# Kernel tuning notes

Measured on AMD Instinct MI355X. Metric: run time of the kernel, lower is better.

Reference implementation:

```python
import jax, jax.numpy as jnp
import numpy as np

T_BINS = 1000  # max_time_bins
N_HEADS = 8
BIN = 64


def _ln(x, g, b):
    m = x.mean(-1, keepdims=True)
    v = ((x - m) ** 2).mean(-1, keepdims=True)
    return (x - m) / jnp.sqrt(v + 1e-5) * g + b


def _time_attn(h, td, mask, wq, bq, wk, bk, wv, bv, wo, bo, temb):
    # h: [B,S,D], td: [B,S] float, mask: [B,S] bool
    B, S, D = h.shape
    dk = D // N_HEADS
    q = (h @ wq + bq).reshape(B, S, N_HEADS, dk)
    k = (h @ wk + bk).reshape(B, S, N_HEADS, dk)
    v = (h @ wv + bv).reshape(B, S, N_HEADS, dk)
    scores = jnp.einsum('bqhd,bkhd->bhqk', q, k) / jnp.sqrt(jnp.float32(dk))
    tb = jnp.clip(td.astype(jnp.int32), 0, T_BINS - 1)
    bias = temb[tb].transpose(0, 2, 1)[:, :, None, :]  # [B,H,1,S], key-position bias
    scores = jnp.where(mask[:, None, None, :], scores + bias, -1e9)
    attn = jax.nn.softmax(scores, axis=-1)
    ctx = jnp.einsum('bhqk,bkhd->bqhd', attn, v).reshape(B, S, D)
    return ctx @ wo + bo


def _forward(x, time_deltas,
             emb_event, emb_rel, emb_abs,
             iq_w, iq_b, ik_w, ik_b, iv_w, iv_b, io_w, io_b, i_temb, i_g, i_bt,
             eq_w, eq_b, ek_w, ek_b, ev_w, ev_b, eo_w, eo_b, e_temb, e_g, e_bt,
             w1, b1, w2, b2):
    B, S = x.shape
    NB = S // BIN  # S chosen as a multiple of bin_size -> no padding
    mask = x != 0  # padding_idx = 0
    ee = emb_event.at[0].set(0.0)  # padding_idx row is zero
    rel_bins = jnp.clip(time_deltas.astype(jnp.int32), 0, T_BINS - 1)
    abs_t = jnp.cumsum(jnp.clip(time_deltas, 0.0, None), axis=1)
    abs_bins = jnp.clip(abs_t.astype(jnp.int32), 0, T_BINS - 1)
    h = ee[x] + emb_rel[rel_bins] + emb_abs[abs_bins]  # [B,S,D]
    D = h.shape[-1]
    # intra-bin attention over [B*NB, BIN]
    hi = h.reshape(B * NB, BIN, D)
    ti = time_deltas.reshape(B * NB, BIN)
    mi = mask.reshape(B * NB, BIN)
    hi = _ln(_time_attn(hi, ti, mi, iq_w, iq_b, ik_w, ik_b, iv_w, iv_b, io_w, io_b, i_temb), i_g, i_bt)
    hi = hi.reshape(B, NB, BIN, D)
    # mean pool per bin over valid tokens
    mb = mask.reshape(B, NB, BIN)
    w = mb[..., None].astype(h.dtype)
    denom = jnp.maximum(w.sum(2), 1.0)
    bin_repr = (hi * w).sum(2) / denom  # [B,NB,D]
    bin_mask = mb.any(2)
    abs_masked = jnp.where(mb, abs_t.reshape(B, NB, BIN), 0.0)
    bin_abs = abs_masked.max(2)
    bin_rel = jnp.concatenate(
        [jnp.zeros((B, 1), h.dtype), jnp.maximum(bin_abs[:, 1:] - bin_abs[:, :-1], 0.0)], axis=1)
    h_inter = _ln(_time_attn(bin_repr, bin_rel, bin_mask,
                             eq_w, eq_b, ek_w, ek_b, ev_w, ev_b, eo_w, eo_b, e_temb), e_g, e_bt)
    last_idx = jnp.clip(bin_mask.sum(1) - 1, 0, None)
    last = h_inter[jnp.arange(B), last_idx]  # [B,D]
    return jax.nn.sigmoid(jax.nn.relu(last @ w1 + b1) @ w2 + b2)  # [B,1]


def setup_inputs() -> dict:
    key = jax.random.key(0)
    ks = jax.random.split(key, 24)
    B, S, D, V = 8, 4096, 512, 20000
    sc = 1.0 / np.sqrt(D)
    f32 = jnp.float32
    inp = {
        'x': jax.random.randint(ks[0], (B, S), 0, V),
        'time_deltas': jax.random.uniform(ks[1], (B, S), f32) * 10.0,
        'emb_event': jax.random.normal(ks[2], (V, D), f32) * 0.02,
        'emb_rel': jax.random.normal(ks[3], (T_BINS, D), f32) * 0.02,
        'emb_abs': jax.random.normal(ks[4], (T_BINS, D), f32) * 0.02,
    }
    names = ['iq', 'ik', 'iv', 'io', 'eq', 'ek', 'ev', 'eo']
    for i, n in enumerate(names):
        inp[n + '_w'] = jax.random.normal(ks[5 + i], (D, D), f32) * sc
        inp[n + '_b'] = jnp.zeros((D,), f32)
    inp['i_temb'] = jax.random.normal(ks[13], (T_BINS, N_HEADS), f32) * 0.02
    inp['e_temb'] = jax.random.normal(ks[14], (T_BINS, N_HEADS), f32) * 0.02
    inp['i_g'] = jnp.ones((D,), f32); inp['i_bt'] = jnp.zeros((D,), f32)
    inp['e_g'] = jnp.ones((D,), f32); inp['e_bt'] = jnp.zeros((D,), f32)
    inp['w1'] = jax.random.normal(ks[15], (D, D // 2), f32) * sc
    inp['b1'] = jnp.zeros((D // 2,), f32)
    inp['w2'] = jax.random.normal(ks[16], (D // 2, 1), f32) * np.sqrt(2.0 / D)
    inp['b2'] = jnp.zeros((1,), f32)
    return inp


def reference(x, time_deltas, emb_event, emb_rel, emb_abs,
              iq_w, iq_b, ik_w, ik_b, iv_w, iv_b, io_w, io_b, i_temb, i_g, i_bt,
              eq_w, eq_b, ek_w, ek_b, ev_w, ev_b, eo_w, eo_b, e_temb, e_g, e_bt,
              w1, b1, w2, b2):
    return _forward(x, time_deltas, emb_event, emb_rel, emb_abs,
                    iq_w, iq_b, ik_w, ik_b, iv_w, iv_b, io_w, io_b, i_temb, i_g, i_bt,
                    eq_w, eq_b, ek_w, ek_b, ev_w, ev_b, eo_w, eo_b, e_temb, e_g, e_bt,
                    w1, b1, w2, b2)
```

## Files before the change

kernel.cpp:

```cpp
#include <hip/hip_runtime.h>


typedef __attribute__((ext_vector_type(8))) short bf16x8;
typedef __attribute__((ext_vector_type(4))) float f32x4;

#define DEVI __device__ __forceinline__

DEVI unsigned short f2bf(float f) {
  union { float f; unsigned u; } v; v.f = f;
  unsigned r = v.u + 0x7FFFu + ((v.u >> 16) & 1u);
  return (unsigned short)(r >> 16);
}
DEVI float bf2f(unsigned short u) {
  union { unsigned u; float f; } v; v.u = ((unsigned)u) << 16; return v.f;
}

#define GLOAD_LDS16(gp, lp) \
  __builtin_amdgcn_global_load_lds((const __attribute__((address_space(1))) void*)(gp), \
                                   (__attribute__((address_space(3))) void*)(lp), 16, 0, 0)

struct TPackArgs { const float* s[8]; unsigned short* d[8]; };

__global__ __launch_bounds__(256) void k_tpack8(TPackArgs args) {
  __shared__ float tile[64][65];
  int mat = blockIdx.x >> 6;
  int tl = blockIdx.x & 63;
  const float* W = args.s[mat];
  unsigned short* Wt = args.d[mat];
  int n0 = (tl & 7) << 6, k0 = (tl >> 3) << 6;
  int t = threadIdx.x, j = t & 63, i0 = t >> 6;
#pragma unroll
  for (int rr = 0; rr < 16; ++rr) {
    int i = rr * 4 + i0;
    tile[i][j] = W[(size_t)(k0 + i) * 512 + n0 + j];
  }
  __syncthreads();
#pragma unroll
  for (int rr = 0; rr < 16; ++rr) {
    int i = rr * 4 + i0;
    Wt[(size_t)(n0 + i) * 512 + k0 + j] = f2bf(tile[j][i]);
  }
}

__global__ __launch_bounds__(256) void k_bias2(const float* __restrict__ a0,
    const float* __restrict__ b0, const float* __restrict__ c0,
    const float* __restrict__ a1, const float* __restrict__ b1, const float* __restrict__ c1,
    float* __restrict__ o0, float* __restrict__ o1) {
  int i = blockIdx.x * 256 + threadIdx.x;
  o0[i] = (i < 512) ? a0[i] : (i < 1024) ? b0[i - 512] : c0[i - 1024];
  o1[i] = (i < 512) ? a1[i] : (i < 1024) ? b1[i - 512] : c1[i - 1024];
}

__global__ __launch_bounds__(64) void k_time(const float* __restrict__ td, const int* __restrict__ x,
    float* __restrict__ abs_t, float* __restrict__ bin_rel, int* __restrict__ bin_mask,
    int* __restrict__ last_idx) {
  int b = blockIdx.x, lane = threadIdx.x;
  const float* row = td + (size_t)b * 4096;
  const int* xr = x + (size_t)b * 4096;
  float* out = abs_t + (size_t)b * 4096;
  __shared__ float babs[64];
  __shared__ int bmask[64];
  float carry = 0.f;
  for (int c = 0; c < 64; ++c) {
    float v = fmaxf(row[c * 64 + lane], 0.f);
#pragma unroll
    for (int off = 1; off < 64; off <<= 1) {
      float n = __shfl_up(v, off, 64);
      if (lane >= off) v += n;
    }
    float a = carry + v;
    out[c * 64 + lane] = a;
    carry += __shfl(v, 63, 64);
    int valid = xr[c * 64 + lane] != 0;
    float am = valid ? a : 0.f;
#pragma unroll
    for (int off = 32; off; off >>= 1) am = fmaxf(am, __shfl_xor(am, off, 64));
    unsigned long long bal = __ballot(valid);
    if (lane == 0) { babs[c] = am; bmask[c] = (bal != 0ULL) ? 1 : 0; }
  }
  __syncthreads();
  float rel = (lane == 0) ? 0.f : fmaxf(babs[lane] - babs[lane - 1], 0.f);
  bin_rel[b * 64 + lane] = rel;
  bin_mask[b * 64 + lane] = bmask[lane];
  unsigned long long bal = __ballot(bmask[lane] != 0);
  if (lane == 0) last_idx[b] = max(__popcll(bal) - 1, 0);
}

__global__ __launch_bounds__(256) void k_embed(const int* __restrict__ x, const float* __restrict__ td,
    const float* __restrict__ abs_t, const float* __restrict__ ee, const float* __restrict__ er,
    const float* __restrict__ ea, unsigned short* __restrict__ h) {
  int t = threadIdx.x;
  int tok = blockIdx.x * 4 + (t >> 6);
  int lane = t & 63;
  int c0 = lane * 8;
  int xi = x[tok];
  int rb = (int)td[tok]; rb = min(max(rb, 0), 999);
  int ab = (int)abs_t[tok]; ab = min(max(ab, 0), 999);
  const f32x4* pr = (const f32x4*)(er + (size_t)rb * 512 + c0);
  const f32x4* pa = (const f32x4*)(ea + (size_t)ab * 512 + c0);
  f32x4 s0 = pr[0] + pa[0];
  f32x4 s1 = pr[1] + pa[1];
  if (xi != 0) {
    const f32x4* pe = (const f32x4*)(ee + (size_t)xi * 512 + c0);
    s0 += pe[0]; s1 += pe[1];
  }
  bf16x8 o;
#pragma unroll
  for (int i = 0; i < 4; ++i) { o[i] = (short)f2bf(s0[i]); o[4 + i] = (short)f2bf(s1[i]); }
  *(bf16x8*)(h + (size_t)tok * 512 + c0) = o;
}

DEVI bf16x8 lds_frag(const unsigned short* buf, int row, int sc) {
  return *(const bf16x8*)&buf[row * 64 + (sc ^ ((row & 7) << 3))];
}

__global__ __launch_bounds__(512, 2) void k_gemm256(const unsigned short* __restrict__ A,
    const unsigned short* __restrict__ Wt, const float* __restrict__ bias,
    unsigned short* __restrict__ Cout, int N, int tiles_n) {
  __shared__ unsigned short lds[2][2][256 * 64];
  int bid = blockIdx.x;
  { int q = (int)gridDim.x >> 3; bid = (bid & 7) * q + (bid >> 3); }
  int by = bid / tiles_n, bx = bid % tiles_n;
  int m0 = by << 8, n0 = bx << 8;
  int t = threadIdx.x;
  int lane = t & 63, w = t >> 6;
  int wm = w >> 2, wn = w & 3;
  int l15 = lane & 15, l4 = lane >> 4;

  auto stage = [&](int kt, int c) {
    int k0 = kt << 6;
#pragma unroll
    for (int l = 0; l < 4; ++l) {
      int idx = l * 512 + t;
      int row = idx >> 3, seg = (idx & 7) ^ (row & 7);
      GLOAD_LDS16(&A[(size_t)(m0 + row) * 512 + k0 + seg * 8], &lds[c][0][idx * 8]);
    }
#pragma unroll
    for (int l = 0; l < 4; ++l) {
      int idx = l * 512 + t;
      int row = idx >> 3, seg = (idx & 7) ^ (row & 7);
      GLOAD_LDS16(&Wt[(size_t)(n0 + row) * 512 + k0 + seg * 8], &lds[c][1][idx * 8]);
    }
  };

  f32x4 acc[8][4] = {};
  stage(0, 0);
  stage(1, 1);
  const int nt = 8;
  for (int kt = 0; kt < nt; ++kt) {
    int c = kt & 1;
    const unsigned short* As = lds[c][0];
    const unsigned short* Bs = lds[c][1];
    if (kt < nt - 1) asm volatile("s_waitcnt vmcnt(8)" ::: "memory");
    else             asm volatile("s_waitcnt vmcnt(0)" ::: "memory");
    __builtin_amdgcn_s_barrier();

    bf16x8 af[4][2], bb[4][2];
#pragma unroll
    for (int i = 0; i < 4; ++i)
#pragma unroll
      for (int ks = 0; ks < 2; ++ks)
        af[i][ks] = lds_frag(As, wm * 128 + i * 16 + l15, ks * 32 + l4 * 8);
#pragma unroll
    for (int j = 0; j < 4; ++j)
#pragma unroll
      for (int ks = 0; ks < 2; ++ks)
        bb[j][ks] = lds_frag(Bs, wn * 64 + j * 16 + l15, ks * 32 + l4 * 8);
    __builtin_amdgcn_sched_barrier(0);
    __builtin_amdgcn_s_barrier();
    asm volatile("s_waitcnt lgkmcnt(0)" ::: "memory");
    __builtin_amdgcn_sched_barrier(0);
    __builtin_amdgcn_s_setprio(1);
#pragma unroll
    for (int i = 0; i < 4; ++i)
#pragma unroll
      for (int j = 0; j < 4; ++j)
#pragma unroll
        for (int ks = 0; ks < 2; ++ks)
          acc[i][j] = __builtin_amdgcn_mfma_f32_16x16x32_bf16(af[i][ks], bb[j][ks], acc[i][j], 0, 0, 0);
    __builtin_amdgcn_s_setprio(0);
    __builtin_amdgcn_s_barrier();

    bf16x8 ah[4][2];
#pragma unroll
    for (int i = 0; i < 4; ++i)
#pragma unroll
      for (int ks = 0; ks < 2; ++ks)
        ah[i][ks] = lds_frag(As, wm * 128 + 64 + i * 16 + l15, ks * 32 + l4 * 8);
    __builtin_amdgcn_sched_barrier(0);
    __builtin_amdgcn_s_barrier();
    asm volatile("s_waitcnt lgkmcnt(0)" ::: "memory");
    __builtin_amdgcn_sched_barrier(0);
    __builtin_amdgcn_s_setprio(1);
#pragma unroll
    for (int i = 0; i < 4; ++i)
#pragma unroll
      for (int j = 0; j < 4; ++j)
#pragma unroll
        for (int ks = 0; ks < 2; ++ks)
          acc[4 + i][j] = __builtin_amdgcn_mfma_f32_16x16x32_bf16(ah[i][ks], bb[j][ks], acc[4 + i][j], 0, 0, 0);
    __builtin_amdgcn_s_setprio(0);
    __builtin_amdgcn_s_barrier();
    if (kt + 2 < nt) stage(kt + 2, c);
  }
#pragma unroll
  for (int i = 0; i < 8; ++i) {
    int rowb = m0 + wm * 128 + i * 16 + (l4 << 2);
#pragma unroll
    for (int j = 0; j < 4; ++j) {
      int col = n0 + wn * 64 + j * 16 + l15;
      float bv = bias[col];
#pragma unroll
      for (int r = 0; r < 4; ++r)
        Cout[(size_t)(rowb + r) * N + col] = f2bf(acc[i][j][r] + bv);
    }
  }
}

__global__ __launch_bounds__(256) void k_gemm(const unsigned short* __restrict__ A,
    const unsigned short* __restrict__ Wt, const float* __restrict__ bias,
    unsigned short* __restrict__ Cout, int N, int tiles_n) {
  __shared__ unsigned short As[128 * 72];
  __shared__ unsigned short Bs[128 * 72];
  int bx = blockIdx.x % tiles_n;
  int by = blockIdx.x / tiles_n;
  int m0 = by << 7, n0 = bx << 7;
  int t = threadIdx.x;
  int lane = t & 63, w = t >> 6;
  int wm = w >> 1, wn = w & 1;
  f32x4 acc[4][4] = {};
  for (int k0 = 0; k0 < 512; k0 += 64) {
    __syncthreads();
#pragma unroll
    for (int i = 0; i < 4; ++i) {
      int idx = t + i * 256;
      int row = idx >> 3, seg = idx & 7;
      *(bf16x8*)&As[row * 72 + seg * 8] = *(const bf16x8*)&A[(size_t)(m0 + row) * 512 + k0 + seg * 8];
      *(bf16x8*)&Bs[row * 72 + seg * 8] = *(const bf16x8*)&Wt[(size_t)(n0 + row) * 512 + k0 + seg * 8];
    }
    __syncthreads();
#pragma unroll
    for (int ks = 0; ks < 2; ++ks) {
      bf16x8 af[4], bb[4];
#pragma unroll
      for (int i = 0; i < 4; ++i) {
        af[i] = *(const bf16x8*)&As[(wm * 64 + i * 16 + (lane & 15)) * 72 + ks * 32 + (lane >> 4) * 8];
        bb[i] = *(const bf16x8*)&Bs[(wn * 64 + i * 16 + (lane & 15)) * 72 + ks * 32 + (lane >> 4) * 8];
      }
#pragma unroll
      for (int i = 0; i < 4; ++i)
#pragma unroll
        for (int j = 0; j < 4; ++j)
          acc[i][j] = __builtin_amdgcn_mfma_f32_16x16x32_bf16(af[i], bb[j], acc[i][j], 0, 0, 0);
    }
  }
#pragma unroll
  for (int i = 0; i < 4; ++i) {
    int rowb = m0 + wm * 64 + i * 16 + ((lane >> 4) << 2);
#pragma unroll
    for (int j = 0; j < 4; ++j) {
      int col = n0 + wn * 64 + j * 16 + (lane & 15);
      float bv = bias[col];
#pragma unroll
      for (int r = 0; r < 4; ++r)
        Cout[(size_t)(rowb + r) * N + col] = f2bf(acc[i][j][r] + bv);
    }
  }
}

__global__ __launch_bounds__(256) void k_attn(const unsigned short* __restrict__ qkv,
    const float* __restrict__ td, const int* __restrict__ validv,
    const float* __restrict__ temb, unsigned short* __restrict__ ctx) {
  __shared__ float bias_s[4][64];
  __shared__ int valid_s[64];
  __shared__ unsigned short P_s[4][64][72];
  __shared__ unsigned short Vt_s[4][64][72];
  int blk = blockIdx.x >> 1, hg = blockIdx.x & 1;
  int t = threadIdx.x, hl = t >> 6, lane = t & 63;
  int h = hg * 4 + hl;
  size_t base = (size_t)blk * 64;
  if (t < 64) {
    valid_s[t] = (validv[base + t] != 0) ? 1 : 0;
    int tb = (int)td[base + t];
    tb = min(max(tb, 0), 999);
#pragma unroll
    for (int hh = 0; hh < 4; ++hh) bias_s[hh][t] = temb[tb * 8 + hg * 4 + hh];
  }
  {
    const unsigned short* vp = qkv + (base + lane) * 1536 + 1024 + h * 64;
#pragma unroll
    for (int f8 = 0; f8 < 8; ++f8) {
      bf16x8 v8 = *(const bf16x8*)(vp + f8 * 8);
#pragma unroll
      for (int j = 0; j < 8; ++j) Vt_s[hl][f8 * 8 + j][lane] = (unsigned short)v8[j];
    }
  }
  __syncthreads();
  bf16x8 qa[2][4], kb[2][4];
#pragma unroll
  for (int ks = 0; ks < 2; ++ks)
#pragma unroll
    for (int i = 0; i < 4; ++i) {
      int row = i * 16 + (lane & 15);
      int kk = ks * 32 + (lane >> 4) * 8;
      qa[ks][i] = *(const bf16x8*)&qkv[(base + row) * 1536 + h * 64 + kk];
      kb[ks][i] = *(const bf16x8*)&qkv[(base + row) * 1536 + 512 + h * 64 + kk];
    }
  f32x4 acc[4][4] = {};
#pragma unroll
  for (int ks = 0; ks < 2; ++ks)
#pragma unroll
    for (int i = 0; i < 4; ++i)
#pragma unroll
      for (int j = 0; j < 4; ++j)
        acc[i][j] = __builtin_amdgcn_mfma_f32_16x16x32_bf16(qa[ks][i], kb[ks][j], acc[i][j], 0, 0, 0);
#pragma unroll
  for (int i = 0; i < 4; ++i) {
#pragma unroll
    for (int r = 0; r < 4; ++r) {
      float sv[4];
#pragma unroll
      for (int j = 0; j < 4; ++j) {
        int key = j * 16 + (lane & 15);
        float s = acc[i][j][r] * 0.125f;
        sv[j] = valid_s[key] ? (s + bias_s[hl][key]) : -1e9f;
      }
      float m = fmaxf(fmaxf(sv[0], sv[1]), fmaxf(sv[2], sv[3]));
#pragma unroll
      for (int off = 1; off < 16; off <<= 1) m = fmaxf(m, __shfl_xor(m, off, 64));
      float p[4], sum = 0.f;
#pragma unroll
      for (int j = 0; j < 4; ++j) { p[j] = __expf(sv[j] - m); sum += p[j]; }
#pragma unroll
      for (int off = 1; off < 16; off <<= 1) sum += __shfl_xor(sum, off, 64);
      float inv = 1.f / sum;
      int row = i * 16 + ((lane >> 4) << 2) + r;
#pragma unroll
      for (int j = 0; j < 4; ++j) P_s[hl][row][j * 16 + (lane & 15)] = f2bf(p[j] * inv);
    }
  }
  __syncthreads();
  f32x4 acc2[4][4] = {};
#pragma unroll
  for (int ks = 0; ks < 2; ++ks) {
    bf16x8 pa[4], vb[4];
    int kk = ks * 32 + (lane >> 4) * 8;
#pragma unroll
    for (int i = 0; i < 4; ++i) {
      pa[i] = *(const bf16x8*)&P_s[hl][i * 16 + (lane & 15)][kk];
      vb[i] = *(const bf16x8*)&Vt_s[hl][i * 16 + (lane & 15)][kk];
    }
#pragma unroll
    for (int i = 0; i < 4; ++i)
#pragma unroll
      for (int j = 0; j < 4; ++j)
        acc2[i][j] = __builtin_amdgcn_mfma_f32_16x16x32_bf16(pa[i], vb[j], acc2[i][j], 0, 0, 0);
  }
#pragma unroll
  for (int i = 0; i < 4; ++i) {
    int rowb = i * 16 + ((lane >> 4) << 2);
#pragma unroll
    for (int j = 0; j < 4; ++j) {
      int col = h * 64 + j * 16 + (lane & 15);
#pragma unroll
      for (int r = 0; r < 4; ++r)
        ctx[(base + rowb + r) * 512 + col] = f2bf(acc2[i][j][r]);
    }
  }
}

__global__ __launch_bounds__(256) void k_lnpool(const unsigned short* __restrict__ X,
    const float* __restrict__ g, const float* __restrict__ bt,
    const int* __restrict__ validv, unsigned short* __restrict__ out) {
  __shared__ float pool_s[4][512];
  __shared__ int cnt_s[4];
  int blk = blockIdx.x;
  int t = threadIdx.x, w = t >> 6, lane = t & 63;
  float gv[8], bv[8];
#pragma unroll
  for (int i = 0; i < 8; ++i) { gv[i] = g[lane * 8 + i]; bv[i] = bt[lane * 8 + i]; }
  float psum[8] = {0.f, 0.f, 0.f, 0.f, 0.f, 0.f, 0.f, 0.f};
  int cnt = 0;
  for (int r0 = 0; r0 < 16; ++r0) {
    int row = blk * 64 + w * 16 + r0;
    bf16x8 xv = *(const bf16x8*)(X + (size_t)row * 512 + lane * 8);
    float xa[8];
#pragma unroll
    for (int i = 0; i < 8; ++i) xa[i] = bf2f((unsigned short)xv[i]);
    float s = 0.f;
#pragma unroll
    for (int i = 0; i < 8; ++i) s += xa[i];
#pragma unroll
    for (int off = 1; off < 64; off <<= 1) s += __shfl_xor(s, off, 64);
    float mean = s * (1.f / 512.f);
    float vsum = 0.f;
#pragma unroll
    for (int i = 0; i < 8; ++i) { float d = xa[i] - mean; vsum += d * d; }
#pragma unroll
    for (int off = 1; off < 64; off <<= 1) vsum += __shfl_xor(vsum, off, 64);
    float rstd = rsqrtf(vsum * (1.f / 512.f) + 1e-5f);
    if (validv[row] != 0) {
      cnt++;
#pragma unroll
      for (int i = 0; i < 8; ++i) psum[i] += (xa[i] - mean) * rstd * gv[i] + bv[i];
    }
  }
#pragma unroll
  for (int i = 0; i < 8; ++i) pool_s[w][lane * 8 + i] = psum[i];
  if (lane == 0) cnt_s[w] = cnt;
  __syncthreads();
  int total = cnt_s[0] + cnt_s[1] + cnt_s[2] + cnt_s[3];
  float denom = fmaxf((float)total, 1.f);
  for (int c = t; c < 512; c += 256) {
    float v = (pool_s[0][c] + pool_s[1][c] + pool_s[2][c] + pool_s[3][c]) / denom;
    out[(size_t)blk * 512 + c] = f2bf(v);
  }
}

__global__ __launch_bounds__(256) void k_final(const unsigned short* __restrict__ proj2,
    const int* __restrict__ last_idx, const float* __restrict__ g, const float* __restrict__ bt,
    const float* __restrict__ w1, const float* __restrict__ b1,
    const float* __restrict__ w2, const float* __restrict__ b2, float* __restrict__ outp) {
  __shared__ float row_s[512];
  __shared__ float red_s[4];
  __shared__ float red2_s[4];
  int b = blockIdx.x, t = threadIdx.x;
  const unsigned short* rp = proj2 + (size_t)(b * 64 + last_idx[b]) * 512;
  float v0 = bf2f(rp[t]), v1 = bf2f(rp[t + 256]);
  float s = v0 + v1;
#pragma unroll
  for (int off = 1; off < 64; off <<= 1) s += __shfl_xor(s, off, 64);
  if ((t & 63) == 0) red_s[t >> 6] = s;
  __syncthreads();
  float mean = (red_s[0] + red_s[1] + red_s[2] + red_s[3]) * (1.f / 512.f);
  float d0 = v0 - mean, d1 = v1 - mean;
  float vs = d0 * d0 + d1 * d1;
#pragma unroll
  for (int off = 1; off < 64; off <<= 1) vs += __shfl_xor(vs, off, 64);
  if ((t & 63) == 0) red2_s[t >> 6] = vs;
  __syncthreads();
  float rstd = rsqrtf((red2_s[0] + red2_s[1] + red2_s[2] + red2_s[3]) * (1.f / 512.f) + 1e-5f);
  row_s[t]       = d0 * rstd * g[t]       + bt[t];
  row_s[t + 256] = d1 * rstd * g[t + 256] + bt[t + 256];
  __syncthreads();
  float acc = b1[t];
  for (int k = 0; k < 512; ++k) acc += row_s[k] * w1[(size_t)k * 256 + t];
  float hv = fmaxf(acc, 0.f) * w2[t];
#pragma unroll
  for (int off = 1; off < 64; off <<= 1) hv += __shfl_xor(hv, off, 64);
  if ((t & 63) == 0) red_s[t >> 6] = hv;
  __syncthreads();
  if (t == 0) {
    float o = red_s[0] + red_s[1] + red_s[2] + red_s[3] + b2[0];
    outp[b] = 1.f / (1.f + __expf(-o));
  }
}

extern "C" void kernel_launch(void* const* d_in, const int* in_sizes, int n_in,
                              void* d_out, int out_size, void* d_ws, size_t ws_size,
                              hipStream_t stream) {
  const int*   x    = (const int*)d_in[0];
  const float* td   = (const float*)d_in[1];
  const float* ee   = (const float*)d_in[2];
  const float* er   = (const float*)d_in[3];
  const float* ea   = (const float*)d_in[4];
  const float* iq_w = (const float*)d_in[5];  const float* iq_b = (const float*)d_in[6];
  const float* ik_w = (const float*)d_in[7];  const float* ik_b = (const float*)d_in[8];
  const float* iv_w = (const float*)d_in[9];  const float* iv_b = (const float*)d_in[10];
  const float* io_w = (const float*)d_in[11]; const float* io_b = (const float*)d_in[12];
  const float* eq_w = (const float*)d_in[13]; const float* eq_b = (const float*)d_in[14];
  const float* ek_w = (const float*)d_in[15]; const float* ek_b = (const float*)d_in[16];
  const float* ev_w = (const float*)d_in[17]; const float* ev_b = (const float*)d_in[18];
  const float* eo_w = (const float*)d_in[19]; const float* eo_b = (const float*)d_in[20];
  const float* i_temb = (const float*)d_in[21];
  const float* e_temb = (const float*)d_in[22];
  const float* i_g  = (const float*)d_in[23]; const float* i_bt = (const float*)d_in[24];
  const float* e_g  = (const float*)d_in[25]; const float* e_bt = (const float*)d_in[26];
  const float* w1   = (const float*)d_in[27]; const float* b1   = (const float*)d_in[28];
  const float* w2   = (const float*)d_in[29]; const float* b2   = (const float*)d_in[30];

  char* ws = (char*)d_ws;
  size_t off = 0;
  auto alloc = [&](size_t nb) { size_t r = off; off += (nb + 255) & ~(size_t)255; return r; };
  float* abs_t    = (float*)(ws + alloc((size_t)32768 * 4));
  float* bin_rel  = (float*)(ws + alloc(512 * 4));
  int*   bin_mask = (int*)(ws + alloc(512 * 4));
  int*   last_idx = (int*)(ws + alloc(64));
  unsigned short* wqkv_i = (unsigned short*)(ws + alloc((size_t)1536 * 512 * 2));
  unsigned short* wo_i   = (unsigned short*)(ws + alloc((size_t)512 * 512 * 2));
  unsigned short* wqkv_e = (unsigned short*)(ws + alloc((size_t)1536 * 512 * 2));
  unsigned short* wo_e   = (unsigned short*)(ws + alloc((size_t)512 * 512 * 2));
  float* bqkv_i = (float*)(ws + alloc(1536 * 4));
  float* bqkv_e = (float*)(ws + alloc(1536 * 4));
  unsigned short* hbuf = (unsigned short*)(ws + alloc((size_t)32768 * 512 * 2));
  char* big = ws + alloc((size_t)32768 * 1536 * 2);
  unsigned short* qkvbuf = (unsigned short*)big;
  unsigned short* projbuf = (unsigned short*)big;
  unsigned short* bin_repr = (unsigned short*)(ws + alloc((size_t)512 * 512 * 2));
  char* small = ws + alloc((size_t)512 * 1536 * 2);
  unsigned short* qkv2 = (unsigned short*)small;
  unsigned short* proj2 = (unsigned short*)small;
  unsigned short* ctx2 = (unsigned short*)(ws + alloc((size_t)512 * 512 * 2));

  TPackArgs tp;
  tp.s[0] = iq_w; tp.d[0] = wqkv_i;
  tp.s[1] = ik_w; tp.d[1] = wqkv_i + (size_t)512 * 512;
  tp.s[2] = iv_w; tp.d[2] = wqkv_i + (size_t)1024 * 512;
  tp.s[3] = io_w; tp.d[3] = wo_i;
  tp.s[4] = eq_w; tp.d[4] = wqkv_e;
  tp.s[5] = ek_w; tp.d[5] = wqkv_e + (size_t)512 * 512;
  tp.s[6] = ev_w; tp.d[6] = wqkv_e + (size_t)1024 * 512;
  tp.s[7] = eo_w; tp.d[7] = wo_e;
  k_tpack8<<<512, 256, 0, stream>>>(tp);
  k_bias2<<<6, 256, 0, stream>>>(iq_b, ik_b, iv_b, eq_b, ek_b, ev_b, bqkv_i, bqkv_e);

  k_time<<<8, 64, 0, stream>>>(td, x, abs_t, bin_rel, bin_mask, last_idx);

  k_embed<<<8192, 256, 0, stream>>>(x, td, abs_t, ee, er, ea, hbuf);

  k_gemm256<<<128 * 6, 512, 0, stream>>>(hbuf, wqkv_i, bqkv_i, qkvbuf, 1536, 6);
  k_attn<<<1024, 256, 0, stream>>>(qkvbuf, td, x, i_temb, hbuf);
  k_gemm256<<<128 * 2, 512, 0, stream>>>(hbuf, wo_i, io_b, projbuf, 512, 2);
  k_lnpool<<<512, 256, 0, stream>>>(projbuf, i_g, i_bt, x, bin_repr);

  k_gemm<<<4 * 12, 256, 0, stream>>>(bin_repr, wqkv_e, bqkv_e, qkv2, 1536, 12);
  k_attn<<<16, 256, 0, stream>>>(qkv2, bin_rel, bin_mask, e_temb, ctx2);
  k_gemm<<<4 * 4, 256, 0, stream>>>(ctx2, wo_e, eo_b, proj2, 512, 4);

  k_final<<<8, 256, 0, stream>>>(proj2, last_idx, e_g, e_bt, w1, b1, w2, b2, (float*)d_out);
}
```

Measured before the change: 266.9 us.

## Deepen GEMM pipeline to 4-stage K=32, fold bias kernel, parallelize time scan

The 256x256 GEMM now uses K-slices of 32 with a four-buffer ring and prefetches three slices ahead. A and B loads are split and issued between the fragment reads and MFMA phases, which removes two barriers per iteration and adds a new LDS swizzle. The bias-concatenation kernel is merged into the weight transpose launch as an extra block, saving one launch. The time-scan kernel switches from 64 serial warp scans to per-lane serial 64-element sums followed by one warp scan, trading fewer shuffles for strided per-lane memory access.

Result: faster. 234.2 us (-12.2%).

```diff
diff --git a/kernel.cpp b/kernel.cpp
--- a/kernel.cpp
+++ b/kernel.cpp
@@ -19,10 +19,20 @@
   __builtin_amdgcn_global_load_lds((const __attribute__((address_space(1))) void*)(gp), \
                                    (__attribute__((address_space(3))) void*)(lp), 16, 0, 0)
 
-struct TPackArgs { const float* s[8]; unsigned short* d[8]; };
+struct TPackArgs { const float* s[8]; unsigned short* d[8];
+                   const float* bs[6]; float* bd[2]; };
 
 __global__ __launch_bounds__(256) void k_tpack8(TPackArgs args) {
   __shared__ float tile[64][65];
+  if (blockIdx.x == 512) {
+    int t = threadIdx.x;
+    for (int i = t; i < 1536; i += 256) {
+      int sel = i >> 9, r = i & 511;
+      args.bd[0][i] = args.bs[sel][r];
+      args.bd[1][i] = args.bs[3 + sel][r];
+    }
+    return;
+  }
   int mat = blockIdx.x >> 6;
   int tl = blockIdx.x & 63;
   const float* W = args.s[mat];
@@ -42,47 +52,32 @@
   }
 }
 
-__global__ __launch_bounds__(256) void k_bias2(const float* __restrict__ a0,
-    const float* __restrict__ b0, const float* __restrict__ c0,
-    const float* __restrict__ a1, const float* __restrict__ b1, const float* __restrict__ c1,
-    float* __restrict__ o0, float* __restrict__ o1) {
-  int i = blockIdx.x * 256 + threadIdx.x;
-  o0[i] = (i < 512) ? a0[i] : (i < 1024) ? b0[i - 512] : c0[i - 1024];
-  o1[i] = (i < 512) ? a1[i] : (i < 1024) ? b1[i - 512] : c1[i - 1024];
-}
-
 __global__ __launch_bounds__(64) void k_time(const float* __restrict__ td, const int* __restrict__ x,
     float* __restrict__ abs_t, float* __restrict__ bin_rel, int* __restrict__ bin_mask,
     int* __restrict__ last_idx) {
   int b = blockIdx.x, lane = threadIdx.x;
-  const float* row = td + (size_t)b * 4096;
-  const int* xr = x + (size_t)b * 4096;
-  float* out = abs_t + (size_t)b * 4096;
-  __shared__ float babs[64];
-  __shared__ int bmask[64];
-  float carry = 0.f;
-  for (int c = 0; c < 64; ++c) {
-    float v = fmaxf(row[c * 64 + lane], 0.f);
-#pragma unroll
-    for (int off = 1; off < 64; off <<= 1) {
-      float n = __shfl_up(v, off, 64);
-      if (lane >= off) v += n;
-    }
-    float a = carry + v;
-    out[c * 64 + lane] = a;
-    carry += __shfl(v, 63, 64);
-    int valid = xr[c * 64 + lane] != 0;
-    float am = valid ? a : 0.f;
-#pragma unroll
-    for (int off = 32; off; off >>= 1) am = fmaxf(am, __shfl_xor(am, off, 64));
-    unsigned long long bal = __ballot(valid);
-    if (lane == 0) { babs[c] = am; bmask[c] = (bal != 0ULL) ? 1 : 0; }
-  }
-  __syncthreads();
-  float rel = (lane == 0) ? 0.f : fmaxf(babs[lane] - babs[lane - 1], 0.f);
-  bin_rel[b * 64 + lane] = rel;
-  bin_mask[b * 64 + lane] = bmask[lane];
-  unsigned long long bal = __ballot(bmask[lane] != 0);
+  const float* row = td + (size_t)b * 4096 + lane * 64;
+  const int*   xr  = x  + (size_t)b * 4096 + lane * 64;
+  float* out = abs_t + (size_t)b * 4096 + lane * 64;
+  float s = 0.f;
+  for (int i = 0; i < 64; ++i) s += fmaxf(row[i], 0.f);
+  float pre = s;
+#pragma unroll
+  for (int off = 1; off < 64; off <<= 1) {
+    float n = __shfl_up(pre, off, 64);
+    if (lane >= off) pre += n;
+  }
+  float a = pre - s;
+  float am = 0.f; int anyv = 0;
+  for (int i = 0; i < 64; ++i) {
+    a += fmaxf(row[i], 0.f);
+    out[i] = a;
+    if (xr[i] != 0) { am = fmaxf(am, a); anyv = 1; }
+  }
+  float prev = __shfl_up(am, 1, 64);
+  bin_rel[b * 64 + lane] = (lane == 0) ? 0.f : fmaxf(am - prev, 0.f);
+  bin_mask[b * 64 + lane] = anyv;
+  unsigned long long bal = __ballot(anyv != 0);
   if (lane == 0) last_idx[b] = max(__popcll(bal) - 1, 0);
 }
 
@@ -110,14 +105,16 @@
   *(bf16x8*)(h + (size_t)tok * 512 + c0) = o;
 }
 
-DEVI bf16x8 lds_frag(const unsigned short* buf, int row, int sc) {
-  return *(const bf16x8*)&buf[row * 64 + (sc ^ ((row & 7) << 3))];
+DEVI bf16x8 lds_frag32(const unsigned short* buf, int r, int g) {
+  int sr = r >> 1;
+  int slot = (((r & 1) << 2) | g) ^ (sr & 7);
+  return *(const bf16x8*)&buf[sr * 64 + slot * 8];
 }
 
 __global__ __launch_bounds__(512, 2) void k_gemm256(const unsigned short* __restrict__ A,
     const unsigned short* __restrict__ Wt, const float* __restrict__ bias,
     unsigned short* __restrict__ Cout, int N, int tiles_n) {
-  __shared__ unsigned short lds[2][2][256 * 64];
+  __shared__ unsigned short lds[4][2][256 * 32];
   int bid = blockIdx.x;
   { int q = (int)gridDim.x >> 3; bid = (bid & 7) * q + (bid >> 3); }
   int by = bid / tiles_n, bx = bid % tiles_n;
@@ -127,45 +124,50 @@
   int wm = w >> 2, wn = w & 3;
   int l15 = lane & 15, l4 = lane >> 4;
 
-  auto stage = [&](int kt, int c) {
-    int k0 = kt << 6;
-#pragma unroll
-    for (int l = 0; l < 4; ++l) {
-      int idx = l * 512 + t;
-      int row = idx >> 3, seg = (idx & 7) ^ (row & 7);
-      GLOAD_LDS16(&A[(size_t)(m0 + row) * 512 + k0 + seg * 8], &lds[c][0][idx * 8]);
-    }
-#pragma unroll
-    for (int l = 0; l < 4; ++l) {
-      int idx = l * 512 + t;
-      int row = idx >> 3, seg = (idx & 7) ^ (row & 7);
-      GLOAD_LDS16(&Wt[(size_t)(n0 + row) * 512 + k0 + seg * 8], &lds[c][1][idx * 8]);
+  auto stageA = [&](int kt) {
+    int k0 = kt << 5;
+    unsigned short* dst = &lds[kt & 3][0][0];
+#pragma unroll
+    for (int l = 0; l < 2; ++l) {
+      int pos = l * 512 + t;
+      int sr = pos >> 3, slot = pos & 7;
+      int gp = slot ^ (sr & 7);
+      int row = sr * 2 + (gp >> 2);
+      GLOAD_LDS16(&A[(size_t)(m0 + row) * 512 + k0 + (gp & 3) * 8], dst + pos * 8);
     }
   };
+  auto stageB = [&](int kt) {
+    int k0 = kt << 5;
+    unsigned short* dst = &lds[kt & 3][1][0];
+#pragma unroll
+    for (int l = 0; l < 2; ++l) {
+      int pos = l * 512 + t;
+      int sr = pos >> 3, slot = pos & 7;
+      int gp = slot ^ (sr & 7);
+      int row = sr * 2 + (gp >> 2);
+      GLOAD_LDS16(&Wt[(size_t)(n0 + row) * 512 + k0 + (gp & 3) * 8], dst + pos * 8);
+    }
+  };
 
   f32x4 acc[8][4] = {};
-  stage(0, 0);
-  stage(1, 1);
-  const int nt = 8;
-  for (int kt = 0; kt < nt; ++kt) {
-    int c = kt & 1;
-    const unsigned short* As = lds[c][0];
-    const unsigned short* Bs = lds[c][1];
-    if (kt < nt - 1) asm volatile("s_waitcnt vmcnt(8)" ::: "memory");
-    else             asm volatile("s_waitcnt vmcnt(0)" ::: "memory");
+  stageA(0); stageB(0);
+  stageA(1); stageB(1);
+  stageA(2); stageB(2);
+
+  for (int kt = 0; kt < 16; ++kt) {
+    if (kt < 14)       asm volatile("s_waitcnt vmcnt(8)" ::: "memory");
+    else if (kt == 14) asm volatile("s_waitcnt vmcnt(4)" ::: "memory");
+    else               asm volatile("s_waitcnt vmcnt(0)" ::: "memory");
     __builtin_amdgcn_s_barrier();
-
-    bf16x8 af[4][2], bb[4][2];
-#pragma unroll
-    for (int i = 0; i < 4; ++i)
-#pragma unroll
-      for (int ks = 0; ks < 2; ++ks)
-        af[i][ks] = lds_frag(As, wm * 128 + i * 16 + l15, ks * 32 + l4 * 8);
-#pragma unroll
-    for (int j = 0; j < 4; ++j)
-#pragma unroll
-      for (int ks = 0; ks < 2; ++ks)
-        bb[j][ks] = lds_frag(Bs, wn * 64 + j * 16 + l15, ks * 32 + l4 * 8);
+    const unsigned short* As = &lds[kt & 3][0][0];
+    const unsigned short* Bs = &lds[kt & 3][1][0];
+
+    bf16x8 af[4], bb[4];
+#pragma unroll
+    for (int i = 0; i < 4; ++i) af[i] = lds_frag32(As, wm * 128 + i * 16 + l15, l4);
+#pragma unroll
+    for (int j = 0; j < 4; ++j) bb[j] = lds_frag32(Bs, wn * 64 + j * 16 + l15, l4);
+    if (kt < 13) stageA(kt + 3);
     __builtin_amdgcn_sched_barrier(0);
     __builtin_amdgcn_s_barrier();
     asm volatile("s_waitcnt lgkmcnt(0)" ::: "memory");
@@ -175,18 +177,13 @@
     for (int i = 0; i < 4; ++i)
 #pragma unroll
       for (int j = 0; j < 4; ++j)
-#pragma unroll
-        for (int ks = 0; ks < 2; ++ks)
-          acc[i][j] = __builtin_amdgcn_mfma_f32_16x16x32_bf16(af[i][ks], bb[j][ks], acc[i][j], 0, 0, 0);
+        acc[i][j] = __builtin_amdgcn_mfma_f32_16x16x32_bf16(af[i], bb[j], acc[i][j], 0, 0, 0);
     __builtin_amdgcn_s_setprio(0);
-    __builtin_amdgcn_s_barrier();
-
-    bf16x8 ah[4][2];
-#pragma unroll
-    for (int i = 0; i < 4; ++i)
-#pragma unroll
-      for (int ks = 0; ks < 2; ++ks)
-        ah[i][ks] = lds_frag(As, wm * 128 + 64 + i * 16 + l15, ks * 32 + l4 * 8);
+
+    bf16x8 ah[4];
+#pragma unroll
+    for (int i = 0; i < 4; ++i) ah[i] = lds_frag32(As, wm * 128 + 64 + i * 16 + l15, l4);
+    if (kt < 13) stageB(kt + 3);
     __builtin_amdgcn_sched_barrier(0);
     __builtin_amdgcn_s_barrier();
     asm volatile("s_waitcnt lgkmcnt(0)" ::: "memory");
@@ -196,12 +193,8 @@
     for (int i = 0; i < 4; ++i)
 #pragma unroll
       for (int j = 0; j < 4; ++j)
-#pragma unroll
-        for (int ks = 0; ks < 2; ++ks)
-          acc[4 + i][j] = __builtin_amdgcn_mfma_f32_16x16x32_bf16(ah[i][ks], bb[j][ks], acc[4 + i][j], 0, 0, 0);
+        acc[4 + i][j] = __builtin_amdgcn_mfma_f32_16x16x32_bf16(ah[i], bb[j], acc[4 + i][j], 0, 0, 0);
     __builtin_amdgcn_s_setprio(0);
-    __builtin_amdgcn_s_barrier();
-    if (kt + 2 < nt) stage(kt + 2, c);
   }
 #pragma unroll
   for (int i = 0; i < 8; ++i) {
@@ -511,8 +504,10 @@
   tp.s[5] = ek_w; tp.d[5] = wqkv_e + (size_t)512 * 512;
   tp.s[6] = ev_w; tp.d[6] = wqkv_e + (size_t)1024 * 512;
   tp.s[7] = eo_w; tp.d[7] = wo_e;
-  k_tpack8<<<512, 256, 0, stream>>>(tp);
-  k_bias2<<<6, 256, 0, stream>>>(iq_b, ik_b, iv_b, eq_b, ek_b, ev_b, bqkv_i, bqkv_e);
+  tp.bs[0] = iq_b; tp.bs[1] = ik_b; tp.bs[2] = iv_b;
+  tp.bs[3] = eq_b; tp.bs[4] = ek_b; tp.bs[5] = ev_b;
+  tp.bd[0] = bqkv_i; tp.bd[1] = bqkv_e;
+  k_tpack8<<<513, 256, 0, stream>>>(tp);
 
   k_time<<<8, 64, 0, stream>>>(td, x, abs_t, bin_rel, bin_mask, last_idx);
 
```
